# Performance work log

Hardware: AMD Instinct MI355X
Metric: run time of the kernel (lower is better)

## Reference

```python
import jax, jax.numpy as jnp
import numpy as np

B, S, D, H = 2, 4096, 512, 8
DK = D // H  # 64

def setup_inputs() -> dict:
    key = jax.random.key(0)
    k1, k2, k3, k4 = jax.random.split(key, 4)
    return {
        "queries": jax.random.normal(k1, (B, S, D), dtype=jnp.float32),
        "keys": jax.random.normal(k2, (B, S, D), dtype=jnp.float32),
        "values": jax.random.normal(k3, (B, S, D), dtype=jnp.float32),
        "W_o": jax.random.normal(k4, (D, D), dtype=jnp.float32) * (1.0 / np.sqrt(D)),
        "b_o": jnp.zeros((D,), dtype=jnp.float32),
    }

def reference(queries, keys, values, W_o, b_o):
    b_s, nq, _ = queries.shape
    nk = keys.shape[1]
    # split heads: (b, s, h, dk) -> (b, h, s, dk)
    q = queries.reshape(b_s, nq, H, DK).transpose(0, 2, 1, 3)
    k = keys.reshape(b_s, nk, H, DK).transpose(0, 2, 1, 3)
    v = values.reshape(b_s, nk, H, DK).transpose(0, 2, 1, 3)
    # full (nq, nk) attention matrix, scaled by sqrt(d_k)
    att = jnp.einsum("bhqd,bhkd->bhqk", q, k) / np.sqrt(DK).astype(np.float32)
    att = jax.nn.softmax(att, axis=-1)  # dropout is identity at inference
    out = jnp.einsum("bhqk,bhkd->bhqd", att, v)
    out = out.transpose(0, 2, 1, 3).reshape(b_s, nq, H * DK)
    return out @ W_o + b_o
```

## Files before the change

kernel.cpp:

```cpp
#include <hip/hip_runtime.h>
#include <hip/hip_bf16.h>

#define Bn 2
#define Sn 4096
#define Dn 512
#define Hn 8

typedef _Float16 f16x8 __attribute__((ext_vector_type(8)));
typedef __fp16 fp16x2 __attribute__((ext_vector_type(2)));
typedef float f32x16 __attribute__((ext_vector_type(16)));
typedef unsigned uint2v __attribute__((ext_vector_type(2)));

#if __has_builtin(__builtin_amdgcn_global_load_lds)
#define HAS_GLL 1
typedef const __attribute__((address_space(1))) unsigned int* gas1_t;
typedef __attribute__((address_space(3))) unsigned int* las3_t;
static __device__ __forceinline__ void ld_lds16(const void* g, void* l) {
    __builtin_amdgcn_global_load_lds((gas1_t)g, (las3_t)l, 16, 0, 0);
}
#else
#define HAS_GLL 0
#endif

static __device__ __forceinline__ unsigned pkh(float a, float b) {
    union { fp16x2 h; unsigned u; } r;
    r.h = __builtin_amdgcn_cvt_pkrtz(a, b);
    return r.u;
}

static __device__ __forceinline__ f16x8 xchg2(unsigned g0x, unsigned g0y,
                                              unsigned g1x, unsigned g1y, int hi) {
    union { unsigned u[4]; f16x8 v; } f;
#if __has_builtin(__builtin_amdgcn_permlane32_swap)
    uint2v rx = __builtin_amdgcn_permlane32_swap(g0x, g1x, false, false);
    uint2v ry = __builtin_amdgcn_permlane32_swap(g0y, g1y, false, false);
    f.u[0] = rx.x; f.u[1] = ry.x; f.u[2] = rx.y; f.u[3] = ry.y;
#else
    int sx = hi ? (int)g0x : (int)g1x;
    int sy = hi ? (int)g0y : (int)g1y;
    int rx = __shfl_xor(sx, 32);
    int ry = __shfl_xor(sy, 32);
    unsigned ox = hi ? g1x : g0x;
    unsigned oy = hi ? g1y : g0y;
    f.u[0] = hi ? (unsigned)rx : ox;
    f.u[1] = hi ? (unsigned)ry : oy;
    f.u[2] = hi ? ox : (unsigned)rx;
    f.u[3] = hi ? oy : (unsigned)ry;
#endif
    return f.v;
}

__global__ __launch_bounds__(256) void prep_kernel(
    const float* __restrict__ K, const float* __restrict__ V, const float* __restrict__ W,
    unsigned short* __restrict__ Kb, unsigned short* __restrict__ Vb,
    unsigned short* __restrict__ Wb) {
    const int vb = blockIdx.x;
    const int tid = threadIdx.x;
    if (vb < 1024) {
        const int kt = vb & 63, bh = vb >> 6;
        const int b = bh >> 3, h = bh & 7;
        unsigned short* dst = Kb + ((size_t)bh * 64 + kt) * 4096;
#pragma unroll
        for (int i = 0; i < 2; ++i) {
            int c = tid + i * 256;
            int f = c >> 6, ln = c & 63;
            int ktile = f >> 2, ks = f & 3;
            int row = ktile * 32 + (ln & 31);
            int dk = ks * 16 + (ln >> 5) * 8;
            const float* src = K + ((size_t)(b * Sn + kt * 64 + row)) * Dn + h * 64 + dk;
            float4 a0 = *(const float4*)src;
            float4 a1 = *(const float4*)(src + 4);
            uint4 o;
            o.x = pkh(a0.x, a0.y); o.y = pkh(a0.z, a0.w);
            o.z = pkh(a1.x, a1.y); o.w = pkh(a1.z, a1.w);
            *(uint4*)(dst + c * 8) = o;
        }
    } else if (vb < 2048) {
        const int u = vb - 1024;
        const int kt = u & 63, bh = u >> 6;
        const int b = bh >> 3, h = bh & 7;
        unsigned short* dst = Vb + ((size_t)bh * 64 + kt) * 4096;
#pragma unroll
        for (int i = 0; i < 2; ++i) {
            int c = tid + i * 256;
            int f = c >> 6, ln = c & 63;
            int dt = f >> 2, ks = f & 3;
            int dk = dt * 32 + (ln & 31);
            int key0 = ks * 16 + (ln >> 5) * 8;
            const float* src = V + ((size_t)(b * Sn + kt * 64 + key0)) * Dn + h * 64 + dk;
            uint4 o;
            o.x = pkh(src[0 * Dn], src[1 * Dn]);
            o.y = pkh(src[2 * Dn], src[3 * Dn]);
            o.z = pkh(src[4 * Dn], src[5 * Dn]);
            o.w = pkh(src[6 * Dn], src[7 * Dn]);
            *(uint4*)(dst + c * 8) = o;
        }
    } else {
        int c = (vb - 2048) * 256 + tid;
        int ln = c & 63, f = c >> 6;
        int ntile = f >> 5, ks = f & 31;
        int n = ntile * 32 + (ln & 31);
        int k0 = ks * 16 + (ln >> 5) * 8;
        uint4 o;
        o.x = pkh(W[(size_t)(k0 + 0) * Dn + n], W[(size_t)(k0 + 1) * Dn + n]);
        o.y = pkh(W[(size_t)(k0 + 2) * Dn + n], W[(size_t)(k0 + 3) * Dn + n]);
        o.z = pkh(W[(size_t)(k0 + 4) * Dn + n], W[(size_t)(k0 + 5) * Dn + n]);
        o.w = pkh(W[(size_t)(k0 + 6) * Dn + n], W[(size_t)(k0 + 7) * Dn + n]);
        *(uint4*)(Wb + c * 8) = o;
    }
}

__global__ __launch_bounds__(256, 2) void attn_kernel(
    const float* __restrict__ Q,
    const unsigned short* __restrict__ Kb,
    const unsigned short* __restrict__ Vb,
    unsigned short* __restrict__ ObA) {
    __shared__ __align__(16) unsigned short KV[16384];

    const int id = blockIdx.x + (blockIdx.y << 6);
    const int qt = (id >> 3) & 63;
    const int bh = (id & 7) + ((id >> 9) << 3);
    const int b = bh >> 3, h = bh & 7;
    const int tid = threadIdx.x;
    const int kg = tid >> 6;
    const int lane = tid & 63;
    const int q = lane & 31;
    const int hi = lane >> 5;
    const float cexp = 0.18033688f;

    f16x8 qf0[4], qf1[4];
    {
        const float* qp0 = Q + ((size_t)(b * Sn + qt * 64 + q)) * Dn + h * 64 + hi * 8;
        const float* qp1 = qp0 + (size_t)32 * Dn;
#pragma unroll
        for (int ks = 0; ks < 4; ++ks) {
            float4 a0 = *(const float4*)(qp0 + ks * 16);
            float4 a1 = *(const float4*)(qp0 + ks * 16 + 4);
            union { unsigned u[4]; f16x8 v; } f;
            f.u[0] = pkh(a0.x * cexp, a0.y * cexp);
            f.u[1] = pkh(a0.z * cexp, a0.w * cexp);
            f.u[2] = pkh(a1.x * cexp, a1.y * cexp);
            f.u[3] = pkh(a1.z * cexp, a1.w * cexp);
            qf0[ks] = f.v;
            a0 = *(const float4*)(qp1 + ks * 16);
            a1 = *(const float4*)(qp1 + ks * 16 + 4);
            f.u[0] = pkh(a0.x * cexp, a0.y * cexp);
            f.u[1] = pkh(a0.z * cexp, a0.w * cexp);
            f.u[2] = pkh(a1.x * cexp, a1.y * cexp);
            f.u[3] = pkh(a1.z * cexp, a1.w * cexp);
            qf1[ks] = f.v;
        }
    }

    f32x16 zf;
#pragma unroll
    for (int r = 0; r < 16; ++r) zf[r] = 0.f;
    f32x16 oacc[2][2];
    oacc[0][0] = zf; oacc[0][1] = zf; oacc[1][0] = zf; oacc[1][1] = zf;
    float l0_ = 0.f, l1_ = 0.f;

    const size_t bhbase = (size_t)bh * 64 * 4096;
    const unsigned short* kB = Kb + bhbase;
    const unsigned short* vB = Vb + bhbase;
    unsigned short* const lb = &KV[kg * 4096];

    for (int it = 0; it < 32; ++it) {
        const int t64 = kg * 16 + (it >> 1);
        const int lohi = it & 1;
        {
            const unsigned short* ks_ = kB + (size_t)t64 * 4096 + lohi * 2048 + lane * 8;
            const unsigned short* vs_ = vB + (size_t)t64 * 4096 + lohi * 1024 + lane * 8;
#if HAS_GLL
            ld_lds16(ks_, lb);          ld_lds16(ks_ + 512, lb + 512);
            ld_lds16(ks_ + 1024, lb + 1024); ld_lds16(ks_ + 1536, lb + 1536);
            ld_lds16(vs_, lb + 2048);   ld_lds16(vs_ + 512, lb + 2560);
            ld_lds16(vs_ + 2048, lb + 3072); ld_lds16(vs_ + 2560, lb + 3584);
            asm volatile("s_waitcnt vmcnt(0)" ::: "memory");
#else
            uint4 a0 = *(const uint4*)(ks_);        uint4 a1 = *(const uint4*)(ks_ + 512);
            uint4 a2 = *(const uint4*)(ks_ + 1024); uint4 a3 = *(const uint4*)(ks_ + 1536);
            uint4 b0 = *(const uint4*)(vs_);        uint4 b1 = *(const uint4*)(vs_ + 512);
            uint4 b2 = *(const uint4*)(vs_ + 2048); uint4 b3 = *(const uint4*)(vs_ + 2560);
            *(uint4*)&lb[lane * 8] = a0;        *(uint4*)&lb[512 + lane * 8] = a1;
            *(uint4*)&lb[1024 + lane * 8] = a2; *(uint4*)&lb[1536 + lane * 8] = a3;
            *(uint4*)&lb[2048 + lane * 8] = b0; *(uint4*)&lb[2560 + lane * 8] = b1;
            *(uint4*)&lb[3072 + lane * 8] = b2; *(uint4*)&lb[3584 + lane * 8] = b3;
            asm volatile("s_waitcnt lgkmcnt(0)" ::: "memory");
#endif
#if __has_builtin(__builtin_amdgcn_sched_barrier)
            __builtin_amdgcn_sched_barrier(0);
#endif
        }

        f32x16 sa0, sa1;
        {
            f16x8 kf = *(const f16x8*)&lb[0 * 512 + lane * 8];
            sa0 = __builtin_amdgcn_mfma_f32_32x32x16_f16(kf, qf0[0], zf, 0, 0, 0);
            sa1 = __builtin_amdgcn_mfma_f32_32x32x16_f16(kf, qf1[0], zf, 0, 0, 0);
#pragma unroll
            for (int ks = 1; ks < 4; ++ks) {
                kf = *(const f16x8*)&lb[ks * 512 + lane * 8];
                sa0 = __builtin_amdgcn_mfma_f32_32x32x16_f16(kf, qf0[ks], sa0, 0, 0, 0);
                sa1 = __builtin_amdgcn_mfma_f32_32x32x16_f16(kf, qf1[ks], sa1, 0, 0, 0);
            }
        }
        unsigned u0[8], u1[8];
        float s0 = 0.f, s1 = 0.f;
#pragma unroll
        for (int j = 0; j < 8; ++j) {
            float ea = __builtin_amdgcn_exp2f(sa0[2 * j]);
            float eb = __builtin_amdgcn_exp2f(sa0[2 * j + 1]);
            s0 += ea + eb;
            u0[j] = pkh(ea, eb);
        }
#pragma unroll
        for (int j = 0; j < 8; ++j) {
            float ea = __builtin_amdgcn_exp2f(sa1[2 * j]);
            float eb = __builtin_amdgcn_exp2f(sa1[2 * j + 1]);
            s1 += ea + eb;
            u1[j] = pkh(ea, eb);
        }
        l0_ += s0; l1_ += s1;

#pragma unroll
        for (int ks2 = 0; ks2 < 2; ++ks2) {
            f16x8 pb0 = xchg2(u0[4 * ks2 + 0], u0[4 * ks2 + 1], u0[4 * ks2 + 2], u0[4 * ks2 + 3], hi);
            f16x8 pb1 = xchg2(u1[4 * ks2 + 0], u1[4 * ks2 + 1], u1[4 * ks2 + 2], u1[4 * ks2 + 3], hi);
            f16x8 va0 = *(const f16x8*)&lb[2048 + ks2 * 512 + lane * 8];
            f16x8 va1 = *(const f16x8*)&lb[3072 + ks2 * 512 + lane * 8];
            oacc[0][0] = __builtin_amdgcn_mfma_f32_32x32x16_f16(va0, pb0, oacc[0][0], 0, 0, 0);
            oacc[0][1] = __builtin_amdgcn_mfma_f32_32x32x16_f16(va1, pb0, oacc[0][1], 0, 0, 0);
            oacc[1][0] = __builtin_amdgcn_mfma_f32_32x32x16_f16(va0, pb1, oacc[1][0], 0, 0, 0);
            oacc[1][1] = __builtin_amdgcn_mfma_f32_32x32x16_f16(va1, pb1, oacc[1][1], 0, 0, 0);
        }
    }

    __syncthreads();
    float* red = (float*)KV;
#pragma unroll
    for (int t = 0; t < 2; ++t) {
        if (kg != 0) {
            float* rp = red + (kg - 1) * 2048;
#pragma unroll
            for (int dt = 0; dt < 2; ++dt)
#pragma unroll
                for (int g = 0; g < 4; ++g) {
                    float4 v;
                    v.x = oacc[t][dt][g * 4 + 0];
                    v.y = oacc[t][dt][g * 4 + 1];
                    v.z = oacc[t][dt][g * 4 + 2];
                    v.w = oacc[t][dt][g * 4 + 3];
                    *(float4*)&rp[(dt * 4 + g) * 256 + lane * 4] = v;
                }
            red[6144 + (kg - 1) * 64 + lane] = t ? l1_ : l0_;
        }
        __syncthreads();
        if (kg == 0) {
#pragma unroll
            for (int slot = 0; slot < 3; ++slot) {
                float* rp = red + slot * 2048;
#pragma unroll
                for (int dt = 0; dt < 2; ++dt)
#pragma unroll
                    for (int g = 0; g < 4; ++g) {
                        float4 v = *(const float4*)&rp[(dt * 4 + g) * 256 + lane * 4];
                        oacc[t][dt][g * 4 + 0] += v.x;
                        oacc[t][dt][g * 4 + 1] += v.y;
                        oacc[t][dt][g * 4 + 2] += v.z;
                        oacc[t][dt][g * 4 + 3] += v.w;
                    }
                float addl = red[6144 + slot * 64 + lane];
                if (t) l1_ += addl; else l0_ += addl;
            }
        }
        __syncthreads();
    }

    if (kg == 0) {
        l0_ += __shfl_xor(l0_, 32);
        l1_ += __shfl_xor(l1_, 32);
#pragma unroll
        for (int t = 0; t < 2; ++t) {
            const float li = 1.f / (t ? l1_ : l0_);
            const int gm = b * 128 + qt * 2 + t;
#pragma unroll
            for (int ksg = 0; ksg < 4; ++ksg) {
                const int dt = ksg >> 1, k2 = ksg & 1;
                unsigned g0x = pkh(oacc[t][dt][8 * k2 + 0] * li, oacc[t][dt][8 * k2 + 1] * li);
                unsigned g0y = pkh(oacc[t][dt][8 * k2 + 2] * li, oacc[t][dt][8 * k2 + 3] * li);
                unsigned g1x = pkh(oacc[t][dt][8 * k2 + 4] * li, oacc[t][dt][8 * k2 + 5] * li);
                unsigned g1y = pkh(oacc[t][dt][8 * k2 + 6] * li, oacc[t][dt][8 * k2 + 7] * li);
                f16x8 frag = xchg2(g0x, g0y, g1x, g1y, hi);
                union { f16x8 v; uint4 u; } fu; fu.v = frag;
                *(uint4*)&ObA[((size_t)(gm * 32 + h * 4 + ksg) * 64 + lane) * 8] = fu.u;
            }
        }
    }
}

__global__ __launch_bounds__(256) void proj_kernel(
    const unsigned short* __restrict__ ObA,
    const unsigned short* __restrict__ Wb,
    const float* __restrict__ bias,
    float* __restrict__ out) {
    __shared__ __align__(16) unsigned short Ash[8192];
    __shared__ __align__(16) unsigned short Wsh[4096];

    const int mt = blockIdx.x;
    const int nt = blockIdx.y;
    const int tid = threadIdx.x;
    const int w = tid >> 6;
    const int lane = tid & 63;
    const int q = lane & 31;
    const int hi = lane >> 5;

    f32x16 acc[2];
#pragma unroll
    for (int t = 0; t < 2; ++t)
#pragma unroll
        for (int r = 0; r < 16; ++r) acc[t][r] = 0.f;

    for (int kt = 0; kt < 8; ++kt) {
        __syncthreads();
#pragma unroll
        for (int i = 0; i < 4; ++i) {
            int ci = (tid >> 6) + i * 4;
            int ml = ci >> 2, ksl = ci & 3;
            *(uint4*)&Ash[ci * 512 + lane * 8] =
                *(const uint4*)(ObA + (((size_t)(mt * 4 + ml) * 32 + kt * 4 + ksl) * 64 + lane) * 8);
        }
#pragma unroll
        for (int i = 0; i < 2; ++i) {
            int ci = (tid >> 6) + i * 4;
            int ntl = ci >> 2, ksl = ci & 3;
            *(uint4*)&Wsh[ci * 512 + lane * 8] =
                *(const uint4*)(Wb + (((size_t)(nt * 2 + ntl) * 32 + kt * 4 + ksl) * 64 + lane) * 8);
        }
        __syncthreads();

#pragma unroll
        for (int ks = 0; ks < 4; ++ks) {
            f16x8 a  = *(const f16x8*)&Ash[(w * 4 + ks) * 512 + lane * 8];
            f16x8 b0 = *(const f16x8*)&Wsh[(0 * 4 + ks) * 512 + lane * 8];
            f16x8 b1 = *(const f16x8*)&Wsh[(4 + ks) * 512 + lane * 8];
            acc[0] = __builtin_amdgcn_mfma_f32_32x32x16_f16(a, b0, acc[0], 0, 0, 0);
            acc[1] = __builtin_amdgcn_mfma_f32_32x32x16_f16(a, b1, acc[1], 0, 0, 0);
        }
    }

#pragma unroll
    for (int ntl = 0; ntl < 2; ++ntl) {
        int col = nt * 64 + ntl * 32 + q;
        float bv = bias[col];
#pragma unroll
        for (int reg = 0; reg < 16; ++reg) {
            int row = mt * 128 + w * 32 + (reg & 3) + 8 * (reg >> 2) + 4 * hi;
            out[(size_t)row * Dn + col] = acc[ntl][reg] + bv;
        }
    }
}

extern "C" void kernel_launch(void* const* d_in, const int* in_sizes, int n_in,
                              void* d_out, int out_size, void* d_ws, size_t ws_size,
                              hipStream_t stream) {
    const float* Q = (const float*)d_in[0];
    const float* K = (const float*)d_in[1];
    const float* V = (const float*)d_in[2];
    const float* W = (const float*)d_in[3];
    const float* bo = (const float*)d_in[4];
    float* out = (float*)d_out;

    char* ws = (char*)d_ws;
    unsigned short* Kb  = (unsigned short*)(ws);
    unsigned short* Vb  = (unsigned short*)(ws + 8388608);
    unsigned short* Wb  = (unsigned short*)(ws + 16777216);
    unsigned short* ObA = (unsigned short*)(ws + 17301504);

    prep_kernel<<<2176, 256, 0, stream>>>(K, V, W, Kb, Vb, Wb);
    attn_kernel<<<dim3(64, 16), 256, 0, stream>>>(Q, Kb, Vb, ObA);
    proj_kernel<<<dim3(64, 8), 256, 0, stream>>>(ObA, Wb, bo, out);
}
```

Baseline: 194.9 us.

## Double-buffer per-wave K/V LDS staging to overlap loads with MFMA compute

Splits the per-wave K/V tile staging into two LDS buffers and issues the next tile's global-to-LDS loads before computing on the current one, waiting only on the older batch with a partial vmcnt. This hides global memory latency behind the QK/softmax/PV work. It doubles the shared memory per block, which could limit occupancy, and relies on in-order wave execution to avoid overwriting a buffer still being read.

Measured after the change: 190.3 us. 1.02x faster.

```diff
diff --git a/kernel.cpp b/kernel.cpp
--- a/kernel.cpp
+++ b/kernel.cpp
@@ -115,7 +115,7 @@
     const unsigned short* __restrict__ Kb,
     const unsigned short* __restrict__ Vb,
     unsigned short* __restrict__ ObA) {
-    __shared__ __align__(16) unsigned short KV[16384];
+    __shared__ __align__(16) unsigned short KV[32768];
 
     const int id = blockIdx.x + (blockIdx.y << 6);
     const int qt = (id >> 3) & 63;
@@ -162,44 +162,45 @@
     const size_t bhbase = (size_t)bh * 64 * 4096;
     const unsigned short* kB = Kb + bhbase;
     const unsigned short* vB = Vb + bhbase;
-    unsigned short* const lb = &KV[kg * 4096];
-
-    for (int it = 0; it < 32; ++it) {
-        const int t64 = kg * 16 + (it >> 1);
-        const int lohi = it & 1;
-        {
-            const unsigned short* ks_ = kB + (size_t)t64 * 4096 + lohi * 2048 + lane * 8;
-            const unsigned short* vs_ = vB + (size_t)t64 * 4096 + lohi * 1024 + lane * 8;
+    unsigned short* const lb = &KV[kg * 8192];
+
 #if HAS_GLL
-            ld_lds16(ks_, lb);          ld_lds16(ks_ + 512, lb + 512);
-            ld_lds16(ks_ + 1024, lb + 1024); ld_lds16(ks_ + 1536, lb + 1536);
-            ld_lds16(vs_, lb + 2048);   ld_lds16(vs_ + 512, lb + 2560);
-            ld_lds16(vs_ + 2048, lb + 3072); ld_lds16(vs_ + 2560, lb + 3584);
-            asm volatile("s_waitcnt vmcnt(0)" ::: "memory");
+#define STAGE(itx, bb) { \
+    const int t64 = kg * 16 + ((itx) >> 1); \
+    const int lohi = (itx) & 1; \
+    unsigned short* dst = lb + (bb) * 4096; \
+    const unsigned short* ks_ = kB + (size_t)t64 * 4096 + lohi * 2048 + lane * 8; \
+    const unsigned short* vs_ = vB + (size_t)t64 * 4096 + lohi * 1024 + lane * 8; \
+    ld_lds16(ks_, dst);          ld_lds16(ks_ + 512, dst + 512); \
+    ld_lds16(ks_ + 1024, dst + 1024); ld_lds16(ks_ + 1536, dst + 1536); \
+    ld_lds16(vs_, dst + 2048);   ld_lds16(vs_ + 512, dst + 2560); \
+    ld_lds16(vs_ + 2048, dst + 3072); ld_lds16(vs_ + 2560, dst + 3584); }
 #else
-            uint4 a0 = *(const uint4*)(ks_);        uint4 a1 = *(const uint4*)(ks_ + 512);
-            uint4 a2 = *(const uint4*)(ks_ + 1024); uint4 a3 = *(const uint4*)(ks_ + 1536);
-            uint4 b0 = *(const uint4*)(vs_);        uint4 b1 = *(const uint4*)(vs_ + 512);
-            uint4 b2 = *(const uint4*)(vs_ + 2048); uint4 b3 = *(const uint4*)(vs_ + 2560);
-            *(uint4*)&lb[lane * 8] = a0;        *(uint4*)&lb[512 + lane * 8] = a1;
-            *(uint4*)&lb[1024 + lane * 8] = a2; *(uint4*)&lb[1536 + lane * 8] = a3;
-            *(uint4*)&lb[2048 + lane * 8] = b0; *(uint4*)&lb[2560 + lane * 8] = b1;
-            *(uint4*)&lb[3072 + lane * 8] = b2; *(uint4*)&lb[3584 + lane * 8] = b3;
-            asm volatile("s_waitcnt lgkmcnt(0)" ::: "memory");
-#endif
-#if __has_builtin(__builtin_amdgcn_sched_barrier)
-            __builtin_amdgcn_sched_barrier(0);
-#endif
-        }
-
+#define STAGE(itx, bb) { \
+    const int t64 = kg * 16 + ((itx) >> 1); \
+    const int lohi = (itx) & 1; \
+    unsigned short* dst = lb + (bb) * 4096; \
+    const unsigned short* ks_ = kB + (size_t)t64 * 4096 + lohi * 2048 + lane * 8; \
+    const unsigned short* vs_ = vB + (size_t)t64 * 4096 + lohi * 1024 + lane * 8; \
+    uint4 a0 = *(const uint4*)(ks_);        uint4 a1 = *(const uint4*)(ks_ + 512); \
+    uint4 a2 = *(const uint4*)(ks_ + 1024); uint4 a3 = *(const uint4*)(ks_ + 1536); \
+    uint4 b0 = *(const uint4*)(vs_);        uint4 b1 = *(const uint4*)(vs_ + 512); \
+    uint4 b2 = *(const uint4*)(vs_ + 2048); uint4 b3 = *(const uint4*)(vs_ + 2560); \
+    *(uint4*)&dst[lane * 8] = a0;        *(uint4*)&dst[512 + lane * 8] = a1; \
+    *(uint4*)&dst[1024 + lane * 8] = a2; *(uint4*)&dst[1536 + lane * 8] = a3; \
+    *(uint4*)&dst[2048 + lane * 8] = b0; *(uint4*)&dst[2560 + lane * 8] = b1; \
+    *(uint4*)&dst[3072 + lane * 8] = b2; *(uint4*)&dst[3584 + lane * 8] = b3; }
+#endif
+
+    auto COMPUTE = [&](const unsigned short* cb) {
         f32x16 sa0, sa1;
         {
-            f16x8 kf = *(const f16x8*)&lb[0 * 512 + lane * 8];
+            f16x8 kf = *(const f16x8*)&cb[0 * 512 + lane * 8];
             sa0 = __builtin_amdgcn_mfma_f32_32x32x16_f16(kf, qf0[0], zf, 0, 0, 0);
             sa1 = __builtin_amdgcn_mfma_f32_32x32x16_f16(kf, qf1[0], zf, 0, 0, 0);
 #pragma unroll
             for (int ks = 1; ks < 4; ++ks) {
-                kf = *(const f16x8*)&lb[ks * 512 + lane * 8];
+                kf = *(const f16x8*)&cb[ks * 512 + lane * 8];
                 sa0 = __builtin_amdgcn_mfma_f32_32x32x16_f16(kf, qf0[ks], sa0, 0, 0, 0);
                 sa1 = __builtin_amdgcn_mfma_f32_32x32x16_f16(kf, qf1[ks], sa1, 0, 0, 0);
             }
@@ -221,19 +222,37 @@
             u1[j] = pkh(ea, eb);
         }
         l0_ += s0; l1_ += s1;
-
 #pragma unroll
         for (int ks2 = 0; ks2 < 2; ++ks2) {
             f16x8 pb0 = xchg2(u0[4 * ks2 + 0], u0[4 * ks2 + 1], u0[4 * ks2 + 2], u0[4 * ks2 + 3], hi);
             f16x8 pb1 = xchg2(u1[4 * ks2 + 0], u1[4 * ks2 + 1], u1[4 * ks2 + 2], u1[4 * ks2 + 3], hi);
-            f16x8 va0 = *(const f16x8*)&lb[2048 + ks2 * 512 + lane * 8];
-            f16x8 va1 = *(const f16x8*)&lb[3072 + ks2 * 512 + lane * 8];
+            f16x8 va0 = *(const f16x8*)&cb[2048 + ks2 * 512 + lane * 8];
+            f16x8 va1 = *(const f16x8*)&cb[3072 + ks2 * 512 + lane * 8];
             oacc[0][0] = __builtin_amdgcn_mfma_f32_32x32x16_f16(va0, pb0, oacc[0][0], 0, 0, 0);
             oacc[0][1] = __builtin_amdgcn_mfma_f32_32x32x16_f16(va1, pb0, oacc[0][1], 0, 0, 0);
             oacc[1][0] = __builtin_amdgcn_mfma_f32_32x32x16_f16(va0, pb1, oacc[1][0], 0, 0, 0);
             oacc[1][1] = __builtin_amdgcn_mfma_f32_32x32x16_f16(va1, pb1, oacc[1][1], 0, 0, 0);
         }
-    }
+    };
+
+    STAGE(0, 0);
+    for (int it = 0; it < 31; ++it) {
+        STAGE(it + 1, (it + 1) & 1);
+#if HAS_GLL
+        asm volatile("s_waitcnt vmcnt(8)" ::: "memory");
+#else
+        asm volatile("s_waitcnt lgkmcnt(0)" ::: "memory");
+#endif
+#if __has_builtin(__builtin_amdgcn_sched_barrier)
+        __builtin_amdgcn_sched_barrier(0);
+#endif
+        COMPUTE(lb + (it & 1) * 4096);
+    }
+    asm volatile("s_waitcnt vmcnt(0) lgkmcnt(0)" ::: "memory");
+#if __has_builtin(__builtin_amdgcn_sched_barrier)
+    __builtin_amdgcn_sched_barrier(0);
+#endif
+    COMPUTE(lb + (31 & 1) * 4096);
 
     __syncthreads();
     float* red = (float*)KV;
```
